# Optimization experiments

Hardware: AMD Instinct MI355X
Metric: run time of the kernel (lower is better)

## Reference

```python
import jax, jax.numpy as jnp
import numpy as np

B, T, D, H = 2, 2048, 1024, 16
HD = D // H            # head dim = 64
WINDOW = 512           # sliding-window size
EPS = 1e-6
ROPE_BASE = 10000.0


def setup_inputs() -> dict:
    key = jax.random.key(0)
    ks = jax.random.split(key, 5)
    s = 0.02  # init scale for dense kernels
    return {
        "x": jax.random.normal(ks[0], (B, T, D), jnp.float32),
        "Wq": jax.random.normal(ks[1], (D, D), jnp.float32) * s,
        "Wk": jax.random.normal(ks[2], (D, D), jnp.float32) * s,
        "Wv": jax.random.normal(ks[3], (D, D), jnp.float32) * s,
        "Wo": jax.random.normal(ks[4], (D, D), jnp.float32) * s,
        "q_scale": jnp.ones((HD,), jnp.float32),
        "k_scale": jnp.ones((HD,), jnp.float32),
        "sink_logit": jnp.zeros((H,), jnp.float32),
    }


def _rmsnorm(x, scale):
    # x: [..., HD]
    var = jnp.mean(jnp.square(x), axis=-1, keepdims=True)
    return x * jax.lax.rsqrt(var + EPS) * scale


def _rope(x):
    # x: [B, H, T, HD]; standard rotate-half RoPE over the full head dim
    half = HD // 2
    inv_freq = 1.0 / (ROPE_BASE ** (jnp.arange(0, HD, 2, dtype=jnp.float32) / HD))  # [half]
    t = jnp.arange(T, dtype=jnp.float32)
    freqs = t[:, None] * inv_freq[None, :]                # [T, half]
    emb = jnp.concatenate([freqs, freqs], axis=-1)        # [T, HD]
    cos = jnp.cos(emb)[None, None]                        # [1,1,T,HD]
    sin = jnp.sin(emb)[None, None]
    x1, x2 = x[..., :half], x[..., half:]
    rot = jnp.concatenate([-x2, x1], axis=-1)
    return x * cos + rot * sin


def reference(x, Wq, Wk, Wv, Wo, q_scale, k_scale, sink_logit):
    # projections -> [B, T, H, HD]
    q = (x @ Wq).reshape(B, T, H, HD)
    k = (x @ Wk).reshape(B, T, H, HD)
    v = (x @ Wv).reshape(B, T, H, HD)
    # QK RMSNorm over head dim
    q = _rmsnorm(q, q_scale)
    k = _rmsnorm(k, k_scale)
    # -> [B, H, T, HD], then RoPE
    q = _rope(q.transpose(0, 2, 1, 3))
    k = _rope(k.transpose(0, 2, 1, 3))
    v = v.transpose(0, 2, 1, 3)
    # causal sliding-window mask
    idx = jnp.arange(T)
    rel = idx[None, :] - idx[:, None]                     # key - query
    mask = ((rel <= 0) & (rel > -WINDOW))[None, None]     # [1,1,T,T]
    scale = HD ** (-0.5)
    scores = jnp.einsum('bhtd,bhsd->bhts', q, k) * scale
    scores = jnp.where(mask, scores, -jnp.inf)
    # sink-augmented softmax: append per-head sink logit to denominator
    sink = jnp.broadcast_to(sink_logit.reshape(1, H, 1, 1), (B, H, T, 1))
    aug = jnp.concatenate([scores.astype(jnp.float32), sink.astype(jnp.float32)], axis=-1)
    weights = jax.nn.softmax(aug, axis=-1)[..., :T].astype(scores.dtype)
    out = jnp.einsum('bhts,bhsd->bhtd', weights, v)
    out = out.transpose(0, 2, 1, 3).reshape(B, T, D)
    return out @ Wo
```

## Files before the change

kernel.cpp:

```cpp
#include <hip/hip_runtime.h>
#include <math.h>

#define CB 2
#define CT 2048
#define CD 1024
#define CH 16
#define CHD 64
#define CWINDOW 512

typedef __bf16 bf16x8 __attribute__((ext_vector_type(8)));
typedef float floatx4 __attribute__((ext_vector_type(4)));

__device__ __forceinline__ unsigned short f2bf(float f) {
  union { float f; unsigned int u; } v;
  v.f = f;
  unsigned int u = v.u;
  u += 0x7fffu + ((u >> 16) & 1u);
  return (unsigned short)(u >> 16);
}
__device__ __forceinline__ unsigned short f2bf_trunc(float f) {
  union { float f; unsigned int u; } v;
  v.f = f;
  return (unsigned short)(v.u >> 16);
}
__device__ __forceinline__ float bf2f(unsigned int h) {
  union { unsigned int u; float f; } v;
  v.u = h << 16;
  return v.f;
}

__global__ __launch_bounds__(256) void cvt_all(const float* __restrict__ x,
                                               const float* __restrict__ Wq,
                                               const float* __restrict__ Wk,
                                               const float* __restrict__ Wv,
                                               const float* __restrict__ Wo,
                                               unsigned short* __restrict__ xb,
                                               unsigned short* __restrict__ WqT,
                                               unsigned short* __restrict__ WkT,
                                               unsigned short* __restrict__ WvT,
                                               unsigned short* __restrict__ WoT) {
  const int z = blockIdx.z;
  if (z < 4) {
    const float* W = z == 0 ? Wq : z == 1 ? Wk : z == 2 ? Wv : Wo;
    unsigned short* Wt = z == 0 ? WqT : z == 1 ? WkT : z == 2 ? WvT : WoT;
    __shared__ float tile[64][65];
    const int k0 = blockIdx.x * 64, n0 = blockIdx.y * 64;
    const int c = threadIdx.x & 63, r4 = threadIdx.x >> 6;
#pragma unroll
    for (int i = 0; i < 16; ++i) {
      int r = i * 4 + r4;
      tile[r][c] = W[(size_t)(k0 + r) * CD + n0 + c];
    }
    __syncthreads();
#pragma unroll
    for (int i = 0; i < 16; ++i) {
      int r = i * 4 + r4;
      Wt[(size_t)(n0 + r) * CD + k0 + c] = f2bf(tile[c][r]);
    }
  } else {
    const int idx = (z - 4) * 256 + blockIdx.y * 16 + blockIdx.x;
    const int i = idx * 256 + threadIdx.x;
    float4 a = ((const float4*)x)[i * 2];
    float4 b = ((const float4*)x)[i * 2 + 1];
    uint4 o;
    o.x = (unsigned int)f2bf(a.x) | ((unsigned int)f2bf(a.y) << 16);
    o.y = (unsigned int)f2bf(a.z) | ((unsigned int)f2bf(a.w) << 16);
    o.z = (unsigned int)f2bf(b.x) | ((unsigned int)f2bf(b.y) << 16);
    o.w = (unsigned int)f2bf(b.z) | ((unsigned int)f2bf(b.w) << 16);
    ((uint4*)xb)[i] = o;
  }
}

__device__ __forceinline__ void async16(const unsigned short* g, unsigned short* l) {
  __builtin_amdgcn_global_load_lds(
      (const __attribute__((address_space(1))) unsigned int*)g,
      (__attribute__((address_space(3))) unsigned int*)l, 16, 0, 0);
}

template <int MODE, int BM>
__device__ __forceinline__ void mfma_gemm_body(const unsigned short* __restrict__ A,
                                               const unsigned short* __restrict__ Bt,
                                               void* __restrict__ Cout,
                                               const float* __restrict__ scale,
                                               float oscale) {
  constexpr int K = CD;
  constexpr int MT = BM / 32;
  __shared__ unsigned short As[BM * 32];
  __shared__ unsigned short Bs[128 * 32];
  const int tid = threadIdx.x;
  const int wave = tid >> 6, lane = tid & 63;
  const int m0 = blockIdx.x * BM, n0 = blockIdx.y * 128;
  const int mq = (wave & 1) * (BM / 2), nq = (wave >> 1) * 64;

  floatx4 acc[MT][4] = {};
  const int srow = lane >> 2;
  const int skc = (lane & 3) * 8;
  const int fr = lane & 15;
  const int fk = (lane >> 4) * 8;

  for (int k0 = 0; k0 < K; k0 += 32) {
    __syncthreads();
#pragma unroll
    for (int it = 0; it < BM / 64; ++it) {
      const int sub = wave * (BM / 64) + it;
      const int row = sub * 16 + srow;
      async16(A + (size_t)(m0 + row) * K + k0 + skc, &As[sub * 512]);
    }
#pragma unroll
    for (int it = 0; it < 2; ++it) {
      const int sub = wave * 2 + it;
      const int row = sub * 16 + srow;
      async16(Bt + (size_t)(n0 + row) * K + k0 + skc, &Bs[sub * 512]);
    }
    __syncthreads();
    bf16x8 af[MT], bg[4];
#pragma unroll
    for (int mt = 0; mt < MT; ++mt)
      af[mt] = *(const bf16x8*)&As[(mq + mt * 16 + fr) * 32 + fk];
#pragma unroll
    for (int nt = 0; nt < 4; ++nt)
      bg[nt] = *(const bf16x8*)&Bs[(nq + nt * 16 + fr) * 32 + fk];
#pragma unroll
    for (int mt = 0; mt < MT; ++mt)
#pragma unroll
      for (int nt = 0; nt < 4; ++nt)
        acc[mt][nt] = __builtin_amdgcn_mfma_f32_16x16x32_bf16(af[mt], bg[nt], acc[mt][nt], 0, 0, 0);
  }

  if (MODE == 1) {
    const int c = lane & 15;
    const int g = lane >> 4;
    const int hh = (n0 + nq) >> 6;
    const float kf = -0.2878231366242557f;
    const float inv0 = __expf((float)c * kf);
    const float inv1 = __expf((float)(16 + c) * kf);
    float sc[4];
#pragma unroll
    for (int nt = 0; nt < 4; ++nt) sc[nt] = scale[nt * 16 + c];
#pragma unroll
    for (int mt = 0; mt < MT; ++mt) {
#pragma unroll
      for (int i = 0; i < 4; ++i) {
        const int m = m0 + mq + mt * 16 + g * 4 + i;
        const int b = m >> 11, t = m & (CT - 1);
        float v0 = acc[mt][0][i], v1 = acc[mt][1][i];
        float v2 = acc[mt][2][i], v3 = acc[mt][3][i];
        float ss = v0 * v0 + v1 * v1 + v2 * v2 + v3 * v3;
#pragma unroll
        for (int off = 8; off > 0; off >>= 1) ss += __shfl_xor(ss, off);
        const float rs = rsqrtf(ss * (1.0f / 64.0f) + 1e-6f);
        v0 *= rs * sc[0];
        v1 *= rs * sc[1];
        v2 *= rs * sc[2];
        v3 *= rs * sc[3];
        const float tf = (float)t;
        const float a0 = tf * inv0, a1 = tf * inv1;
        const float s0 = __sinf(a0), c0 = __cosf(a0);
        const float s1 = __sinf(a1), c1 = __cosf(a1);
        unsigned short* dst = (unsigned short*)Cout + ((size_t)(b * CH + hh) * CT + t) * CHD;
        ushort4 o;
        o.x = f2bf((v0 * c0 - v2 * s0) * oscale);
        o.y = f2bf((v1 * c1 - v3 * s1) * oscale);
        o.z = f2bf((v2 * c0 + v0 * s0) * oscale);
        o.w = f2bf((v3 * c1 + v1 * s1) * oscale);
        *(ushort4*)&dst[4 * c] = o;
      }
    }
  } else {
#pragma unroll
    for (int mt = 0; mt < MT; ++mt) {
#pragma unroll
      for (int nt = 0; nt < 4; ++nt) {
        const int col = n0 + nq + nt * 16 + (lane & 15);
        if (MODE == 2) {
          const int mb = m0 + mq + mt * 16 + (lane >> 4) * 4;
          const int b = mb >> 11, t = mb & (CT - 1);
          const int h = col >> 6, d = col & 63;
          ushort4 o;
          o.x = f2bf(acc[mt][nt][0]);
          o.y = f2bf(acc[mt][nt][1]);
          o.z = f2bf(acc[mt][nt][2]);
          o.w = f2bf(acc[mt][nt][3]);
          *(ushort4*)&((unsigned short*)Cout)[((size_t)(b * CH + h) * CHD + d) * CT + t] = o;
        } else {
#pragma unroll
          for (int i = 0; i < 4; ++i) {
            const int m = m0 + mq + mt * 16 + (lane >> 4) * 4 + i;
            ((float*)Cout)[(size_t)m * CD + col] = acc[mt][nt][i];
          }
        }
      }
    }
  }
}

__global__ __launch_bounds__(256, 3) void gemm_qkv_mfma(const unsigned short* __restrict__ xb,
                                                        const unsigned short* __restrict__ WqT,
                                                        const unsigned short* __restrict__ WkT,
                                                        const unsigned short* __restrict__ WvT,
                                                        unsigned short* __restrict__ Qh,
                                                        unsigned short* __restrict__ Kh,
                                                        unsigned short* __restrict__ Vt,
                                                        const float* __restrict__ q_scale,
                                                        const float* __restrict__ k_scale) {
  if (blockIdx.z == 2) {
    mfma_gemm_body<2, 128>(xb, WvT, Vt, nullptr, 1.0f);
  } else if (blockIdx.z == 0) {
    mfma_gemm_body<1, 128>(xb, WqT, Qh, q_scale, 0.125f);
  } else {
    mfma_gemm_body<1, 128>(xb, WkT, Kh, k_scale, 1.0f);
  }
}

__global__ __launch_bounds__(256, 3) void gemm_out_mfma(const unsigned short* __restrict__ AO,
                                                        const unsigned short* __restrict__ WoT,
                                                        float* __restrict__ out) {
  mfma_gemm_body<0, 64>(AO, WoT, out, nullptr, 1.0f);
}

__device__ __forceinline__ bf16x8 frag64(const unsigned short* base, int row, int ks, int lane) {
  const int phys = (((ks << 2) + (lane >> 4)) ^ (lane & 7)) << 3;
  return *(const bf16x8*)&base[(row << 6) + phys];
}

__global__ __launch_bounds__(256, 2) void attn_mfma(const unsigned short* __restrict__ Qh,
                                                    const unsigned short* __restrict__ Kh,
                                                    const unsigned short* __restrict__ Vt,
                                                    const float* __restrict__ sink_logit,
                                                    unsigned short* __restrict__ AO) {
  __shared__ unsigned short Qs[128 * 64];
  __shared__ unsigned short Ks[2][64 * 64];
  __shared__ unsigned short Vs[2][64 * 64];
  __shared__ unsigned short Ps[128 * 72];

  const int tid = threadIdx.x;
  const int w = tid >> 6, lane = tid & 63;
  const int qb = blockIdx.x, bh = blockIdx.y;
  const int b = bh >> 4, h = bh & 15;
  const int q0 = qb * 128;
  const unsigned short* Qb = Qh + (size_t)bh * CT * CHD;
  const unsigned short* Kb = Kh + (size_t)bh * CT * CHD;
  const unsigned short* Vb = Vt + (size_t)bh * CHD * CT;

  const int l7 = lane & 7, l8 = lane >> 3;
  const int sx8 = (l7 ^ l8) * 8;

  const int kb_lo = (qb >= 4) ? (qb * 2 - 8) : 0;
  const int kb_hi = qb * 2 + 1;

#pragma unroll
  for (int s = 0; s < 4; ++s) {
    const int slab = w * 4 + s;
    async16(Qb + (size_t)(q0 + slab * 8 + l8) * CHD + sx8, &Qs[slab * 512]);
  }
#pragma unroll
  for (int s = 0; s < 2; ++s) {
    const int slab = w * 2 + s;
    const int row = slab * 8 + l8;
    async16(Kb + (size_t)(kb_lo * 64 + row) * CHD + sx8, &Ks[0][slab * 512]);
    async16(Vb + (size_t)row * CT + kb_lo * 64 + sx8, &Vs[0][slab * 512]);
  }
  __syncthreads();

  bf16x8 qf[2][2];
#pragma unroll
  for (int nt = 0; nt < 2; ++nt)
#pragma unroll
    for (int ks = 0; ks < 2; ++ks)
      qf[nt][ks] = frag64(Qs, w * 32 + nt * 16 + (lane & 15), ks, lane);

  floatx4 acc[4][2] = {};
  float lsum[2] = {0.f, 0.f};
  const int qw = q0 + w * 32;

  int cur = 0;
  for (int kb = kb_lo; kb <= kb_hi; ++kb) {
    if (kb < kb_hi) {
#pragma unroll
      for (int s = 0; s < 2; ++s) {
        const int slab = w * 2 + s;
        const int row = slab * 8 + l8;
        async16(Kb + (size_t)((kb + 1) * 64 + row) * CHD + sx8, &Ks[cur ^ 1][slab * 512]);
        async16(Vb + (size_t)row * CT + (kb + 1) * 64 + sx8, &Vs[cur ^ 1][slab * 512]);
      }
    }

    const int kmin = kb * 64, kmax = kb * 64 + 63;
    if (!(kmin > qw + 31 || kmax <= qw - CWINDOW)) {
      const unsigned short* Kc = Ks[cur];
      const unsigned short* Vc = Vs[cur];

      floatx4 st[4][2] = {};
#pragma unroll
      for (int ks = 0; ks < 2; ++ks) {
        bf16x8 kf[4];
#pragma unroll
        for (int mt = 0; mt < 4; ++mt)
          kf[mt] = frag64(Kc, mt * 16 + (lane & 15), ks, lane);
        __builtin_amdgcn_s_setprio(1);
#pragma unroll
        for (int mt = 0; mt < 4; ++mt)
#pragma unroll
          for (int nt = 0; nt < 2; ++nt)
            st[mt][nt] = __builtin_amdgcn_mfma_f32_16x16x32_bf16(kf[mt], qf[nt][ks], st[mt][nt], 0, 0, 0);
        __builtin_amdgcn_s_setprio(0);
      }

      const bool need_c = (kmax > qw);
      const bool need_w = (kmin <= qw + 31 - CWINDOW);
#pragma unroll
      for (int mt = 0; mt < 4; ++mt) {
#pragma unroll
        for (int nt = 0; nt < 2; ++nt) {
          const int s_base = kb * 64 + mt * 16 + (lane >> 4) * 4;
          const int t_g = q0 + w * 32 + nt * 16 + (lane & 15);
          ushort4 pk;
          float psum = 0.f;
#pragma unroll
          for (int i = 0; i < 4; ++i) {
            float sv = st[mt][nt][i];
            if (need_c || need_w) {
              const int s_g = s_base + i;
              const bool ok = (!need_c || (s_g <= t_g)) && (!need_w || (s_g > t_g - CWINDOW));
              sv = ok ? sv : -INFINITY;
            }
            const unsigned short pb = f2bf_trunc(__expf(sv));
            ((unsigned short*)&pk)[i] = pb;
            psum += bf2f(pb);
          }
          lsum[nt] += psum;
          const int qrow = w * 32 + nt * 16 + (lane & 15);
          const int scol = mt * 16 + (lane >> 4) * 4;
          *(ushort4*)&Ps[qrow * 72 + scol] = pk;
        }
      }

#pragma unroll
      for (int ks = 0; ks < 2; ++ks) {
        bf16x8 vf[4], pf[2];
#pragma unroll
        for (int mt = 0; mt < 4; ++mt)
          vf[mt] = frag64(Vc, mt * 16 + (lane & 15), ks, lane);
#pragma unroll
        for (int nt = 0; nt < 2; ++nt) {
          const int qrow = w * 32 + nt * 16 + (lane & 15);
          pf[nt] = *(const bf16x8*)&Ps[qrow * 72 + ks * 32 + (lane >> 4) * 8];
        }
        __builtin_amdgcn_s_setprio(1);
#pragma unroll
        for (int mt = 0; mt < 4; ++mt)
#pragma unroll
          for (int nt = 0; nt < 2; ++nt)
            acc[mt][nt] = __builtin_amdgcn_mfma_f32_16x16x32_bf16(vf[mt], pf[nt], acc[mt][nt], 0, 0, 0);
        __builtin_amdgcn_s_setprio(0);
      }
    }

    asm volatile("s_waitcnt vmcnt(0)" ::: "memory");
    __builtin_amdgcn_s_barrier();
    cur ^= 1;
  }

  const float sinkw = __expf(sink_logit[h]);
  float inv[2];
#pragma unroll
  for (int nt = 0; nt < 2; ++nt) {
    float l = lsum[nt];
    l += __shfl_xor(l, 16);
    l += __shfl_xor(l, 32);
    inv[nt] = 1.0f / (l + sinkw);
  }
#pragma unroll
  for (int mt = 0; mt < 4; ++mt) {
#pragma unroll
    for (int nt = 0; nt < 2; ++nt) {
      const int t_g = q0 + w * 32 + nt * 16 + (lane & 15);
      const int d0 = mt * 16 + (lane >> 4) * 4;
      ushort4 o;
      o.x = f2bf(acc[mt][nt][0] * inv[nt]);
      o.y = f2bf(acc[mt][nt][1] * inv[nt]);
      o.z = f2bf(acc[mt][nt][2] * inv[nt]);
      o.w = f2bf(acc[mt][nt][3] * inv[nt]);
      *(ushort4*)&AO[(size_t)(b * CT + t_g) * CD + h * CHD + d0] = o;
    }
  }
}

extern "C" void kernel_launch(void* const* d_in, const int* in_sizes, int n_in,
                              void* d_out, int out_size, void* d_ws, size_t ws_size,
                              hipStream_t stream) {
  (void)in_sizes;
  (void)n_in;
  (void)out_size;
  (void)ws_size;
  const float* x = (const float*)d_in[0];
  const float* Wq = (const float*)d_in[1];
  const float* Wk = (const float*)d_in[2];
  const float* Wv = (const float*)d_in[3];
  const float* Wo = (const float*)d_in[4];
  const float* q_scale = (const float*)d_in[5];
  const float* k_scale = (const float*)d_in[6];
  const float* sink = (const float*)d_in[7];
  float* out = (float*)d_out;

  const size_t per = (size_t)CB * CH * CT * CHD;
  unsigned short* Qh = (unsigned short*)d_ws;
  unsigned short* Kh = Qh + per;
  unsigned short* Vt = Kh + per;
  unsigned short* AO = Vt + per;
  unsigned short* xb = AO + per;
  unsigned short* WqT = xb + per;
  unsigned short* WkT = WqT + (size_t)CD * CD;
  unsigned short* WvT = WkT + (size_t)CD * CD;
  unsigned short* WoT = WvT + (size_t)CD * CD;

  dim3 blk(256);
  cvt_all<<<dim3(16, 16, 12), blk, 0, stream>>>(x, Wq, Wk, Wv, Wo, xb, WqT, WkT, WvT, WoT);
  gemm_qkv_mfma<<<dim3(32, 8, 3), blk, 0, stream>>>(xb, WqT, WkT, WvT, Qh, Kh, Vt, q_scale, k_scale);
  attn_mfma<<<dim3(CT / 128, CB * CH), blk, 0, stream>>>(Qh, Kh, Vt, sink, AO);
  gemm_out_mfma<<<dim3(64, 8), blk, 0, stream>>>(AO, WoT, out);
}
```

Measured before the change: 168.1 us.

## Widen GEMM K-tile to 64 and remap block indices for cache locality

The shared MFMA GEMM body now stages 64-wide K slices of A and B in LDS and runs two MFMA sub-steps per stage. This halves the number of barrier and load rounds across the K loop, at the cost of twice the LDS per block. The QKV, output-projection and attention kernels also remap the flat block index so that neighbouring blocks share A rows or K/V heads, aiming for better L2 reuse. The unswizzled 128-byte row stride in LDS may add bank conflicts on fragment reads.

```diff
diff --git a/kernel.cpp b/kernel.cpp
--- a/kernel.cpp
+++ b/kernel.cpp
@@ -82,49 +82,49 @@
                                                const unsigned short* __restrict__ Bt,
                                                void* __restrict__ Cout,
                                                const float* __restrict__ scale,
-                                               float oscale) {
+                                               float oscale, int m0, int n0) {
   constexpr int K = CD;
   constexpr int MT = BM / 32;
-  __shared__ unsigned short As[BM * 32];
-  __shared__ unsigned short Bs[128 * 32];
+  __shared__ unsigned short As[BM * 64];
+  __shared__ unsigned short Bs[128 * 64];
   const int tid = threadIdx.x;
   const int wave = tid >> 6, lane = tid & 63;
-  const int m0 = blockIdx.x * BM, n0 = blockIdx.y * 128;
   const int mq = (wave & 1) * (BM / 2), nq = (wave >> 1) * 64;
 
   floatx4 acc[MT][4] = {};
-  const int srow = lane >> 2;
-  const int skc = (lane & 3) * 8;
+  const int srow = lane >> 3;
+  const int skc = (lane & 7) * 8;
   const int fr = lane & 15;
   const int fk = (lane >> 4) * 8;
 
-  for (int k0 = 0; k0 < K; k0 += 32) {
+  for (int k0 = 0; k0 < K; k0 += 64) {
     __syncthreads();
 #pragma unroll
-    for (int it = 0; it < BM / 64; ++it) {
-      const int sub = wave * (BM / 64) + it;
-      const int row = sub * 16 + srow;
-      async16(A + (size_t)(m0 + row) * K + k0 + skc, &As[sub * 512]);
-    }
-#pragma unroll
-    for (int it = 0; it < 2; ++it) {
-      const int sub = wave * 2 + it;
-      const int row = sub * 16 + srow;
-      async16(Bt + (size_t)(n0 + row) * K + k0 + skc, &Bs[sub * 512]);
+    for (int it = 0; it < BM / 32; ++it) {
+      const int s = wave * (BM / 32) + it;
+      async16(A + (size_t)(m0 + s * 8 + srow) * K + k0 + skc, &As[s * 512]);
+    }
+#pragma unroll
+    for (int it = 0; it < 4; ++it) {
+      const int s = wave * 4 + it;
+      async16(Bt + (size_t)(n0 + s * 8 + srow) * K + k0 + skc, &Bs[s * 512]);
     }
     __syncthreads();
-    bf16x8 af[MT], bg[4];
-#pragma unroll
-    for (int mt = 0; mt < MT; ++mt)
-      af[mt] = *(const bf16x8*)&As[(mq + mt * 16 + fr) * 32 + fk];
-#pragma unroll
-    for (int nt = 0; nt < 4; ++nt)
-      bg[nt] = *(const bf16x8*)&Bs[(nq + nt * 16 + fr) * 32 + fk];
-#pragma unroll
-    for (int mt = 0; mt < MT; ++mt)
+#pragma unroll
+    for (int ks = 0; ks < 2; ++ks) {
+      bf16x8 af[MT], bg[4];
+#pragma unroll
+      for (int mt = 0; mt < MT; ++mt)
+        af[mt] = *(const bf16x8*)&As[(mq + mt * 16 + fr) * 64 + ks * 32 + fk];
 #pragma unroll
       for (int nt = 0; nt < 4; ++nt)
-        acc[mt][nt] = __builtin_amdgcn_mfma_f32_16x16x32_bf16(af[mt], bg[nt], acc[mt][nt], 0, 0, 0);
+        bg[nt] = *(const bf16x8*)&Bs[(nq + nt * 16 + fr) * 64 + ks * 32 + fk];
+#pragma unroll
+      for (int mt = 0; mt < MT; ++mt)
+#pragma unroll
+        for (int nt = 0; nt < 4; ++nt)
+          acc[mt][nt] = __builtin_amdgcn_mfma_f32_16x16x32_bf16(af[mt], bg[nt], acc[mt][nt], 0, 0, 0);
+    }
   }
 
   if (MODE == 1) {
@@ -203,19 +203,26 @@
                                                         unsigned short* __restrict__ Vt,
                                                         const float* __restrict__ q_scale,
                                                         const float* __restrict__ k_scale) {
-  if (blockIdx.z == 2) {
-    mfma_gemm_body<2, 128>(xb, WvT, Vt, nullptr, 1.0f);
-  } else if (blockIdx.z == 0) {
-    mfma_gemm_body<1, 128>(xb, WqT, Qh, q_scale, 0.125f);
+  const unsigned int L = blockIdx.x + 32u * blockIdx.y + 256u * blockIdx.z;
+  const int m0 = (int)((L >> 3) & 31u) * 128;
+  const int n0 = (int)(L & 7u) * 128;
+  const int bz = (int)(L >> 8);
+  if (bz == 2) {
+    mfma_gemm_body<2, 128>(xb, WvT, Vt, nullptr, 1.0f, m0, n0);
+  } else if (bz == 0) {
+    mfma_gemm_body<1, 128>(xb, WqT, Qh, q_scale, 0.125f, m0, n0);
   } else {
-    mfma_gemm_body<1, 128>(xb, WkT, Kh, k_scale, 1.0f);
+    mfma_gemm_body<1, 128>(xb, WkT, Kh, k_scale, 1.0f, m0, n0);
   }
 }
 
 __global__ __launch_bounds__(256, 3) void gemm_out_mfma(const unsigned short* __restrict__ AO,
                                                         const unsigned short* __restrict__ WoT,
                                                         float* __restrict__ out) {
-  mfma_gemm_body<0, 64>(AO, WoT, out, nullptr, 1.0f);
+  const unsigned int L = blockIdx.x + 64u * blockIdx.y;
+  const int m0 = (int)(L >> 3) * 64;
+  const int n0 = (int)(L & 7u) * 128;
+  mfma_gemm_body<0, 64>(AO, WoT, out, nullptr, 1.0f, m0, n0);
 }
 
 __device__ __forceinline__ bf16x8 frag64(const unsigned short* base, int row, int ks, int lane) {
@@ -235,7 +242,9 @@
 
   const int tid = threadIdx.x;
   const int w = tid >> 6, lane = tid & 63;
-  const int qb = blockIdx.x, bh = blockIdx.y;
+  const unsigned int L = blockIdx.x + 16u * blockIdx.y;
+  const int qb = (int)((L >> 3) & 15u);
+  const int bh = (int)(L & 7u) * 4 + (int)(L >> 7);
   const int b = bh >> 4, h = bh & 15;
   const int q0 = qb * 128;
   const unsigned short* Qb = Qh + (size_t)bh * CT * CHD;
```

After: 191.5 us. 13.9% more time.
